# Kernel optimization log

Hardware: AMD Instinct MI355X
Metric: run time of the kernel (lower is better)

Reference implementation:

```python
import jax, jax.numpy as jnp
import numpy as np

NHEAD = 16
HEAD_DIM = 64
EMBED_DIM = NHEAD * HEAD_DIM  # 1024
U, R, L, M = 2048, 256, 1024, 512


def setup_inputs() -> dict:
    key = jax.random.key(0)
    ks = jax.random.split(key, 11)
    D = EMBED_DIM
    inp = {
        "utterance": jax.random.normal(ks[0], (U, 1, D), jnp.float32),
        "right_context": jax.random.normal(ks[1], (R, 1, D), jnp.float32),
        "memory": jax.random.normal(ks[2], (M, 1, D), jnp.float32),
        "left_context_key": jax.random.normal(ks[3], (L, 1, D), jnp.float32),
        "left_context_val": jax.random.normal(ks[4], (L, 1, D), jnp.float32),
        "Wq": jax.random.normal(ks[5], (D, D), jnp.float32) * 0.02,
        "bq": jax.random.normal(ks[6], (D,), jnp.float32) * 0.02,
        "Wkv": jax.random.normal(ks[7], (2 * D, D), jnp.float32) * 0.02,
        "bkv": jax.random.normal(ks[8], (2 * D,), jnp.float32) * 0.02,
        "Wo": jax.random.normal(ks[9], (D, D), jnp.float32) * 0.02,
        "bo": jax.random.normal(ks[10], (D,), jnp.float32) * 0.02,
    }
    return inp


def reference(utterance, right_context, memory, left_context_key, left_context_val,
              Wq, bq, Wkv, bkv, Wo, bo):
    D = EMBED_DIM
    scaling = HEAD_DIM ** (-0.5)

    # query = Linear([right_context; utterance])  -> (Q, 1, D), Q = R + U
    q_in = jnp.concatenate([right_context, utterance], axis=0)
    query = q_in @ Wq.T + bq

    # key/value = Linear([memory; right_context; utterance]) split in two
    kv_in = jnp.concatenate([memory, right_context, utterance], axis=0)
    kv = kv_in @ Wkv.T + bkv  # (M+R+U, 1, 2D)
    k_new, v_new = kv[..., :D], kv[..., D:]

    # insert cached left-context key/value after [memory; right_context]
    key = jnp.concatenate([k_new[: M + R], left_context_key, k_new[M + R:]], axis=0)
    value = jnp.concatenate([v_new[: M + R], left_context_val, v_new[M + R:]], axis=0)

    Q = U + R
    KV = M + R + L + U
    # (T, 1, D) -> (nhead, T, head_dim)
    q = query.reshape(Q, NHEAD, HEAD_DIM).transpose(1, 0, 2)
    k = key.reshape(KV, NHEAD, HEAD_DIM).transpose(1, 0, 2)
    v = value.reshape(KV, NHEAD, HEAD_DIM).transpose(1, 0, 2)

    weights = jnp.einsum("hqd,hkd->hqk", q * scaling, k)  # (nhead, Q, KV)
    probs = jax.nn.softmax(weights, axis=-1)
    attn = jnp.einsum("hqk,hkd->hqd", probs, v)  # (nhead, Q, head_dim)

    attn = attn.transpose(1, 0, 2).reshape(Q, D)[:, None, :]  # (Q, 1, D)
    out = attn @ Wo.T + bo
    return out, key, value
```

## Files before the change

kernel.cpp:

```cpp
#include <hip/hip_runtime.h>
#include <hip/hip_bf16.h>

#define EMBED   1024
#define NHEADS  16
#define HDIM    64
#define U_LEN   2048
#define R_LEN   256
#define L_LEN   1024
#define M_LEN   512
#define Q_LEN   (U_LEN + R_LEN)
#define KV_LEN  (M_LEN + R_LEN + L_LEN + U_LEN)
#define X_ROWS  (M_LEN + R_LEN + U_LEN)
#define NPART   6
#define KV_PART (KV_LEN / NPART)

typedef __attribute__((ext_vector_type(8))) short short8;
typedef __attribute__((ext_vector_type(4))) float f32x4;
typedef __attribute__((ext_vector_type(16))) float f32x16;

#define QSCALE 0.180336880f

__device__ __forceinline__ void gl2lds16(const __hip_bfloat16* g, __hip_bfloat16* l) {
  __builtin_amdgcn_global_load_lds(
      (const __attribute__((address_space(1))) unsigned int*)g,
      (__attribute__((address_space(3))) unsigned int*)l, 16, 0, 0);
}

__device__ __forceinline__ unsigned pack_bf16(float a, float b) {
  unsigned ua = __builtin_bit_cast(unsigned, a) + 0x8000u;
  unsigned ub = __builtin_bit_cast(unsigned, b) + 0x8000u;
  return (ua >> 16) | (ub & 0xFFFF0000u);
}

__global__ __launch_bounds__(256) void prep_kernel(
    const float* __restrict__ mem, const float* __restrict__ rc,
    const float* __restrict__ utt, const float* __restrict__ lk,
    const float* __restrict__ lv, const float* __restrict__ Wq,
    const float* __restrict__ Wkv, const float* __restrict__ Wo,
    __hip_bfloat16* __restrict__ X, __hip_bfloat16* __restrict__ WB,
    __hip_bfloat16* __restrict__ WoB,
    float* __restrict__ key_out, float* __restrict__ val_out,
    __hip_bfloat16* __restrict__ k_bf, __hip_bfloat16* __restrict__ v_bf) {
  int b = blockIdx.x, tid = threadIdx.x;
  if (b < 2816) {
    int row = b, col = tid * 4;
    const float* src;
    if (row < M_LEN)              src = mem + row * EMBED;
    else if (row < M_LEN + R_LEN) src = rc + (row - M_LEN) * EMBED;
    else                          src = utt + (row - M_LEN - R_LEN) * EMBED;
    float4 v = *reinterpret_cast<const float4*>(src + col);
    __hip_bfloat16* d = X + (size_t)row * EMBED + col;
    d[0] = __float2bfloat16(v.x); d[1] = __float2bfloat16(v.y);
    d[2] = __float2bfloat16(v.z); d[3] = __float2bfloat16(v.w);
  } else if (b < 6912) {
    const float* src; __hip_bfloat16* dst;
    int blk;
    if (b < 3840)      { src = Wq;  dst = WB;                blk = b - 2816; }
    else if (b < 5888) { src = Wkv; dst = WB + 1024 * 1024;  blk = b - 3840; }
    else               { src = Wo;  dst = WoB;               blk = b - 5888; }
    int idx = blk * 1024 + tid * 4;
    float4 v = *reinterpret_cast<const float4*>(src + idx);
    dst[idx + 0] = __float2bfloat16(v.x);
    dst[idx + 1] = __float2bfloat16(v.y);
    dst[idx + 2] = __float2bfloat16(v.z);
    dst[idx + 3] = __float2bfloat16(v.w);
  } else {
    int row = b - 6912, c0 = tid * 4;
    int orow = 768 + row;
    float4 kv4 = *reinterpret_cast<const float4*>(lk + row * EMBED + c0);
    float4 vv4 = *reinterpret_cast<const float4*>(lv + row * EMBED + c0);
    *reinterpret_cast<float4*>(key_out + (size_t)orow * EMBED + c0) = kv4;
    *reinterpret_cast<float4*>(val_out + (size_t)orow * EMBED + c0) = vv4;
    __hip_bfloat16* kd = k_bf + (size_t)orow * EMBED + c0;
    __hip_bfloat16* vd = v_bf + (size_t)orow * EMBED + c0;
    kd[0] = __float2bfloat16(kv4.x); kd[1] = __float2bfloat16(kv4.y);
    kd[2] = __float2bfloat16(kv4.z); kd[3] = __float2bfloat16(kv4.w);
    vd[0] = __float2bfloat16(vv4.x); vd[1] = __float2bfloat16(vv4.y);
    vd[2] = __float2bfloat16(vv4.z); vd[3] = __float2bfloat16(vv4.w);
  }
}

__global__ __launch_bounds__(256) void transpose_kernel(
    const unsigned short* __restrict__ v_bf, unsigned short* __restrict__ vT) {
  __shared__ unsigned short T[64][72];
  int kt = blockIdx.x * 64, d0 = blockIdx.y * 64;
  int t = threadIdx.x;
  int r = t >> 3, c = (t & 7) * 8;
#pragma unroll
  for (int half = 0; half < 2; half++) {
    int kv = r + half * 32;
    short8 v = *reinterpret_cast<const short8*>(v_bf + (size_t)(kt + kv) * EMBED + d0 + c);
#pragma unroll
    for (int j = 0; j < 8; j++) T[c + j][kv] = (unsigned short)v[j];
  }
  __syncthreads();
#pragma unroll
  for (int half = 0; half < 2; half++) {
    int d = r + half * 32;
    *reinterpret_cast<short8*>(vT + (size_t)(d0 + d) * KV_LEN + kt + c) =
        *reinterpret_cast<const short8*>(&T[d][c]);
  }
}

__global__ __launch_bounds__(256) void gemm_qkv(
    const __hip_bfloat16* __restrict__ A, const __hip_bfloat16* __restrict__ B,
    const float* __restrict__ bq, const float* __restrict__ bkv,
    float* __restrict__ key_out, float* __restrict__ val_out,
    __hip_bfloat16* __restrict__ q_bf, __hip_bfloat16* __restrict__ k_bf,
    __hip_bfloat16* __restrict__ v_bf) {
  __shared__ __align__(16) __hip_bfloat16 As[128 * 32];
  __shared__ __align__(16) __hip_bfloat16 Bs[128 * 32];
  const int K = EMBED;
  int tid = threadIdx.x;
  int wave = tid >> 6, lane = tid & 63, quad = lane >> 4, l16 = lane & 15;
  int wm = wave >> 1, wn = wave & 1;
  int mbase = blockIdx.y * 128, nbase = blockIdx.x * 128;

  if (nbase < 1024 && mbase + 128 <= 512) return;

  const __hip_bfloat16* a0 = A + (size_t)(mbase + (tid >> 2)) * K + (tid & 3) * 8;
  const __hip_bfloat16* a1 = a0 + (size_t)64 * K;
  const __hip_bfloat16* b0 = B + (size_t)(nbase + (tid >> 2)) * K + (tid & 3) * 8;
  const __hip_bfloat16* b1 = b0 + (size_t)64 * K;
  __hip_bfloat16* lA0 = As + tid * 8;
  __hip_bfloat16* lA1 = As + (tid + 256) * 8;
  __hip_bfloat16* lB0 = Bs + tid * 8;
  __hip_bfloat16* lB1 = Bs + (tid + 256) * 8;

  f32x4 acc[4][4] = {};
  for (int kt = 0; kt < K; kt += 32) {
    gl2lds16(a0 + kt, lA0);
    gl2lds16(a1 + kt, lA1);
    gl2lds16(b0 + kt, lB0);
    gl2lds16(b1 + kt, lB1);
    __syncthreads();
    short8 af[4], bfr[4];
#pragma unroll
    for (int i = 0; i < 4; i++)
      af[i] = *reinterpret_cast<const short8*>(As + (wm * 64 + i * 16 + l16) * 32 + quad * 8);
#pragma unroll
    for (int j = 0; j < 4; j++)
      bfr[j] = *reinterpret_cast<const short8*>(Bs + (wn * 64 + j * 16 + l16) * 32 + quad * 8);
#pragma unroll
    for (int i = 0; i < 4; i++)
#pragma unroll
      for (int j = 0; j < 4; j++)
        acc[i][j] = __builtin_amdgcn_mfma_f32_16x16x32_bf16(af[i], bfr[j], acc[i][j], 0, 0, 0);
    __syncthreads();
  }

#pragma unroll
  for (int i = 0; i < 4; i++) {
    int rb = mbase + wm * 64 + i * 16 + quad * 4;
#pragma unroll
    for (int j = 0; j < 4; j++) {
      int cg = nbase + wn * 64 + j * 16 + l16;
      float bv = (cg < 1024) ? bq[cg] : bkv[cg - 1024];
#pragma unroll
      for (int reg = 0; reg < 4; reg++) {
        int rg = rb + reg;
        float val = acc[i][j][reg] + bv;
        if (cg < 1024) {
          if (rg >= 512)
            q_bf[(size_t)(rg - 512) * 1024 + cg] = __float2bfloat16(val * QSCALE);
        } else {
          int orow = (rg < 768) ? rg : rg + 1024;
          if (cg < 2048) {
            int cc = cg - 1024;
            key_out[(size_t)orow * 1024 + cc] = val;
            k_bf[(size_t)orow * 1024 + cc] = __float2bfloat16(val);
          } else {
            int cc = cg - 2048;
            val_out[(size_t)orow * 1024 + cc] = val;
            v_bf[(size_t)orow * 1024 + cc] = __float2bfloat16(val);
          }
        }
      }
    }
  }
}

__global__ __launch_bounds__(256) void gemm_out(
    const __hip_bfloat16* __restrict__ A, const __hip_bfloat16* __restrict__ B,
    const float* __restrict__ bias, float* __restrict__ outf) {
  __shared__ __align__(16) __hip_bfloat16 As[64 * 32];
  __shared__ __align__(16) __hip_bfloat16 Bs[128 * 32];
  const int K = EMBED, N = EMBED;
  int tid = threadIdx.x;
  int wave = tid >> 6, lane = tid & 63, quad = lane >> 4, l16 = lane & 15;
  int wm = wave >> 1, wn = wave & 1;
  int mbase = blockIdx.y * 64, nbase = blockIdx.x * 128;

  const __hip_bfloat16* a0 = A + (size_t)(mbase + (tid >> 2)) * K + (tid & 3) * 8;
  const __hip_bfloat16* b0 = B + (size_t)(nbase + (tid >> 2)) * K + (tid & 3) * 8;
  const __hip_bfloat16* b1 = b0 + (size_t)64 * K;
  __hip_bfloat16* lA0 = As + tid * 8;
  __hip_bfloat16* lB0 = Bs + tid * 8;
  __hip_bfloat16* lB1 = Bs + (tid + 256) * 8;

  f32x4 acc[2][4] = {};
  for (int kt = 0; kt < K; kt += 32) {
    gl2lds16(a0 + kt, lA0);
    gl2lds16(b0 + kt, lB0);
    gl2lds16(b1 + kt, lB1);
    __syncthreads();
    short8 af[2], bfr[4];
#pragma unroll
    for (int i = 0; i < 2; i++)
      af[i] = *reinterpret_cast<const short8*>(As + (wm * 32 + i * 16 + l16) * 32 + quad * 8);
#pragma unroll
    for (int j = 0; j < 4; j++)
      bfr[j] = *reinterpret_cast<const short8*>(Bs + (wn * 64 + j * 16 + l16) * 32 + quad * 8);
#pragma unroll
    for (int i = 0; i < 2; i++)
#pragma unroll
      for (int j = 0; j < 4; j++)
        acc[i][j] = __builtin_amdgcn_mfma_f32_16x16x32_bf16(af[i], bfr[j], acc[i][j], 0, 0, 0);
    __syncthreads();
  }

#pragma unroll
  for (int i = 0; i < 2; i++) {
    int rb = mbase + wm * 32 + i * 16 + quad * 4;
#pragma unroll
    for (int j = 0; j < 4; j++) {
      int cg = nbase + wn * 64 + j * 16 + l16;
      float bv = bias[cg];
#pragma unroll
      for (int reg = 0; reg < 4; reg++)
        outf[(size_t)(rb + reg) * N + cg] = acc[i][j][reg] + bv;
    }
  }
}

__global__ __launch_bounds__(256, 4) void attn_kernel(
    const __hip_bfloat16* __restrict__ q_bf, const __hip_bfloat16* __restrict__ k_bf,
    const __hip_bfloat16* __restrict__ vT,
    __hip_bfloat16* __restrict__ o_part, float* __restrict__ lsum) {
  __shared__ __align__(16) __hip_bfloat16 Ks[64][72];
  __shared__ __align__(16) __hip_bfloat16 VTs[64][72];
  int tid = threadIdx.x;
  int w = tid >> 6, lane = tid & 63, l31 = lane & 31, h2 = lane >> 5;
  int h = blockIdx.y, part = blockIdx.z;
  int qbase = blockIdx.x * 128;
  int qg = qbase + w * 32 + l31;

  short8 Qf[4];
#pragma unroll
  for (int ks = 0; ks < 4; ks++)
    Qf[ks] = *reinterpret_cast<const short8*>(
        q_bf + (size_t)qg * EMBED + h * HDIM + ks * 16 + h2 * 8);

  f32x16 ot[2] = {};
  float l_run = 0.f;

  int sr = tid >> 3, sc = (tid & 7) * 8;
  const int kv0 = part * KV_PART;

  for (int kt = kv0; kt < kv0 + KV_PART; kt += 64) {
#pragma unroll
    for (int half = 0; half < 2; half++) {
      int r = sr + half * 32;
      *reinterpret_cast<short8*>(&Ks[r][sc]) =
          *reinterpret_cast<const short8*>(k_bf + (size_t)(kt + r) * EMBED + h * HDIM + sc);
      *reinterpret_cast<short8*>(&VTs[r][sc]) =
          *reinterpret_cast<const short8*>(vT + (size_t)(h * HDIM + r) * KV_LEN + kt + sc);
    }
    __syncthreads();

#pragma unroll
    for (int kvs = 0; kvs < 2; kvs++) {
      f32x16 s = {};
#pragma unroll
      for (int ks = 0; ks < 4; ks++) {
        short8 ak = *reinterpret_cast<const short8*>(&Ks[kvs * 32 + l31][ks * 16 + h2 * 8]);
        s = __builtin_amdgcn_mfma_f32_32x32x16_bf16(ak, Qf[ks], s, 0, 0, 0);
      }
      unsigned u[4][2];
#pragma unroll
      for (int g = 0; g < 4; g++) {
        float p0 = exp2f(s[4 * g + 0]), p1 = exp2f(s[4 * g + 1]);
        float p2 = exp2f(s[4 * g + 2]), p3 = exp2f(s[4 * g + 3]);
        l_run += (p0 + p1) + (p2 + p3);
        u[g][0] = pack_bf16(p0, p1);
        u[g][1] = pack_bf16(p2, p3);
      }
#pragma unroll
      for (int half = 0; half < 2; half++) {
        int c = kvs * 2 + half;
        int gA = 2 * half, gB = 2 * half + 1;
        unsigned s0 = h2 ? u[gA][0] : u[gB][0];
        unsigned s1 = h2 ? u[gA][1] : u[gB][1];
        unsigned r0 = __shfl_xor(s0, 32, 64);
        unsigned r1 = __shfl_xor(s1, 32, 64);
        uint4 fr;
        fr.x = h2 ? r0 : u[gA][0];
        fr.y = h2 ? r1 : u[gA][1];
        fr.z = h2 ? u[gB][0] : r0;
        fr.w = h2 ? u[gB][1] : r1;
        short8 pf = __builtin_bit_cast(short8, fr);
#pragma unroll
        for (int ds = 0; ds < 2; ds++) {
          short8 av = *reinterpret_cast<const short8*>(&VTs[ds * 32 + l31][c * 16 + h2 * 8]);
          ot[ds] = __builtin_amdgcn_mfma_f32_32x32x16_bf16(av, pf, ot[ds], 0, 0, 0);
        }
      }
    }
    __syncthreads();
  }

  l_run += __shfl_xor(l_run, 32, 64);
  float inv = 1.0f / l_run;

  size_t orow = (size_t)part * Q_LEN + qg;
#pragma unroll
  for (int ds = 0; ds < 2; ds++)
#pragma unroll
    for (int g = 0; g < 4; g++) {
      uint2 pk;
      pk.x = pack_bf16(ot[ds][4 * g + 0] * inv, ot[ds][4 * g + 1] * inv);
      pk.y = pack_bf16(ot[ds][4 * g + 2] * inv, ot[ds][4 * g + 3] * inv);
      *reinterpret_cast<uint2*>(
          o_part + orow * 1024 + h * HDIM + ds * 32 + g * 8 + h2 * 4) = pk;
    }
  if (lane < 32)
    lsum[orow * NHEADS + h] = l_run;
}

__global__ __launch_bounds__(256) void merge_kernel(
    const __hip_bfloat16* __restrict__ o_part, const float* __restrict__ lsum,
    __hip_bfloat16* __restrict__ attn_bf) {
  int q = blockIdx.x;
  int c = threadIdx.x * 4;
  int h = c >> 6;
  float wt[NPART], L = 0.f;
#pragma unroll
  for (int p = 0; p < NPART; p++) {
    wt[p] = lsum[((size_t)p * Q_LEN + q) * NHEADS + h];
    L += wt[p];
  }
  float invL = 1.0f / L;
  float acc[4] = {0.f, 0.f, 0.f, 0.f};
#pragma unroll
  for (int p = 0; p < NPART; p++) {
    __hip_bfloat16 v[4];
    *reinterpret_cast<uint2*>(v) =
        *reinterpret_cast<const uint2*>(o_part + ((size_t)p * Q_LEN + q) * 1024 + c);
#pragma unroll
    for (int j = 0; j < 4; j++) acc[j] += wt[p] * __bfloat162float(v[j]);
  }
  uint2 pk;
  pk.x = pack_bf16(acc[0] * invL, acc[1] * invL);
  pk.y = pack_bf16(acc[2] * invL, acc[3] * invL);
  *reinterpret_cast<uint2*>(attn_bf + (size_t)q * 1024 + c) = pk;
}


extern "C" void kernel_launch(void* const* d_in, const int* in_sizes, int n_in,
                              void* d_out, int out_size, void* d_ws, size_t ws_size,
                              hipStream_t stream) {
  const float* utt = (const float*)d_in[0];
  const float* rc  = (const float*)d_in[1];
  const float* mem = (const float*)d_in[2];
  const float* lk  = (const float*)d_in[3];
  const float* lv  = (const float*)d_in[4];
  const float* Wq  = (const float*)d_in[5];
  const float* bq  = (const float*)d_in[6];
  const float* Wkv = (const float*)d_in[7];
  const float* bkv = (const float*)d_in[8];
  const float* Wo  = (const float*)d_in[9];
  const float* bo  = (const float*)d_in[10];

  float* out_f   = (float*)d_out;
  float* key_out = out_f + Q_LEN * EMBED;
  float* val_out = key_out + KV_LEN * EMBED;

  char* ws = (char*)d_ws;
  size_t off = 0;
  __hip_bfloat16* X_bf   = (__hip_bfloat16*)(ws + off); off += (size_t)X_ROWS * EMBED * 2;
  __hip_bfloat16* WB_bf  = (__hip_bfloat16*)(ws + off); off += (size_t)3 * EMBED * EMBED * 2;
  __hip_bfloat16* Wo_bf  = (__hip_bfloat16*)(ws + off); off += (size_t)EMBED * EMBED * 2;
  __hip_bfloat16* q_bf   = (__hip_bfloat16*)(ws + off); off += (size_t)Q_LEN * EMBED * 2;
  __hip_bfloat16* k_bf   = (__hip_bfloat16*)(ws + off); off += (size_t)KV_LEN * EMBED * 2;
  __hip_bfloat16* vT_bf  = (__hip_bfloat16*)(ws + off); off += (size_t)EMBED * KV_LEN * 2;
  __hip_bfloat16* o_part = (__hip_bfloat16*)(ws + off); off += (size_t)NPART * Q_LEN * EMBED * 2;
  __hip_bfloat16* attn_bf = X_bf;
  float* lsum = (float*)WB_bf;
  __hip_bfloat16* v_bf = o_part;
  (void)off; (void)ws_size; (void)in_sizes; (void)n_in; (void)out_size;

  prep_kernel<<<7936, 256, 0, stream>>>(mem, rc, utt, lk, lv, Wq, Wkv, Wo,
                                        X_bf, WB_bf, Wo_bf,
                                        key_out, val_out, k_bf, v_bf);
  gemm_qkv<<<dim3(3 * EMBED / 128, X_ROWS / 128), 256, 0, stream>>>(
      X_bf, WB_bf, bq, bkv, key_out, val_out, q_bf, k_bf, v_bf);
  transpose_kernel<<<dim3(KV_LEN / 64, EMBED / 64), 256, 0, stream>>>(
      (const unsigned short*)v_bf, (unsigned short*)vT_bf);
  attn_kernel<<<dim3(Q_LEN / 128, NHEADS, NPART), 256, 0, stream>>>(
      q_bf, k_bf, vT_bf, o_part, lsum);
  merge_kernel<<<Q_LEN, 256, 0, stream>>>(o_part, lsum, attn_bf);
  gemm_out<<<dim3(EMBED / 128, Q_LEN / 64), 256, 0, stream>>>(
      attn_bf, Wo_bf, bo, out_f);
}
```

Before: 243.0 us.

## Retile GEMMs with BK=64 XOR-swizzled LDS and split-K output projection

```diff
diff --git a/kernel.cpp b/kernel.cpp
--- a/kernel.cpp
+++ b/kernel.cpp
@@ -108,44 +108,48 @@
     float* __restrict__ key_out, float* __restrict__ val_out,
     __hip_bfloat16* __restrict__ q_bf, __hip_bfloat16* __restrict__ k_bf,
     __hip_bfloat16* __restrict__ v_bf) {
-  __shared__ __align__(16) __hip_bfloat16 As[128 * 32];
-  __shared__ __align__(16) __hip_bfloat16 Bs[128 * 32];
+  __shared__ __align__(16) __hip_bfloat16 As[128 * 64];
+  __shared__ __align__(16) __hip_bfloat16 Bs[64 * 64];
   const int K = EMBED;
   int tid = threadIdx.x;
   int wave = tid >> 6, lane = tid & 63, quad = lane >> 4, l16 = lane & 15;
   int wm = wave >> 1, wn = wave & 1;
-  int mbase = blockIdx.y * 128, nbase = blockIdx.x * 128;
+  int mbase = blockIdx.y * 128, nbase = blockIdx.x * 64;
 
   if (nbase < 1024 && mbase + 128 <= 512) return;
 
-  const __hip_bfloat16* a0 = A + (size_t)(mbase + (tid >> 2)) * K + (tid & 3) * 8;
-  const __hip_bfloat16* a1 = a0 + (size_t)64 * K;
-  const __hip_bfloat16* b0 = B + (size_t)(nbase + (tid >> 2)) * K + (tid & 3) * 8;
-  const __hip_bfloat16* b1 = b0 + (size_t)64 * K;
-  __hip_bfloat16* lA0 = As + tid * 8;
-  __hip_bfloat16* lA1 = As + (tid + 256) * 8;
-  __hip_bfloat16* lB0 = Bs + tid * 8;
-  __hip_bfloat16* lB1 = Bs + (tid + 256) * 8;
-
-  f32x4 acc[4][4] = {};
-  for (int kt = 0; kt < K; kt += 32) {
-    gl2lds16(a0 + kt, lA0);
-    gl2lds16(a1 + kt, lA1);
-    gl2lds16(b0 + kt, lB0);
-    gl2lds16(b1 + kt, lB1);
-    __syncthreads();
-    short8 af[4], bfr[4];
-#pragma unroll
-    for (int i = 0; i < 4; i++)
-      af[i] = *reinterpret_cast<const short8*>(As + (wm * 64 + i * 16 + l16) * 32 + quad * 8);
-#pragma unroll
-    for (int j = 0; j < 4; j++)
-      bfr[j] = *reinterpret_cast<const short8*>(Bs + (wn * 64 + j * 16 + l16) * 32 + quad * 8);
-#pragma unroll
-    for (int i = 0; i < 4; i++)
-#pragma unroll
-      for (int j = 0; j < 4; j++)
-        acc[i][j] = __builtin_amdgcn_mfma_f32_16x16x32_bf16(af[i], bfr[j], acc[i][j], 0, 0, 0);
+  int srow = tid >> 3;
+  int scol = ((tid & 7) ^ (srow & 7)) * 8;
+  const __hip_bfloat16* aG = A + (size_t)(mbase + srow) * K + scol;
+  const __hip_bfloat16* bG = B + (size_t)(nbase + srow) * K + scol;
+  int swz = l16 & 7;
+
+  f32x4 acc[4][2] = {};
+  for (int kt = 0; kt < K; kt += 64) {
+    gl2lds16(aG + kt, As + tid * 8);
+    gl2lds16(aG + (size_t)32 * K + kt, As + (tid + 256) * 8);
+    gl2lds16(aG + (size_t)64 * K + kt, As + (tid + 512) * 8);
+    gl2lds16(aG + (size_t)96 * K + kt, As + (tid + 768) * 8);
+    gl2lds16(bG + kt, Bs + tid * 8);
+    gl2lds16(bG + (size_t)32 * K + kt, Bs + (tid + 256) * 8);
+    __syncthreads();
+#pragma unroll
+    for (int ks = 0; ks < 2; ks++) {
+      short8 af[4], bfr[2];
+#pragma unroll
+      for (int i = 0; i < 4; i++)
+        af[i] = *reinterpret_cast<const short8*>(
+            As + (wm * 64 + i * 16 + l16) * 64 + ((ks * 4 + quad) ^ swz) * 8);
+#pragma unroll
+      for (int j = 0; j < 2; j++)
+        bfr[j] = *reinterpret_cast<const short8*>(
+            Bs + (wn * 32 + j * 16 + l16) * 64 + ((ks * 4 + quad) ^ swz) * 8);
+#pragma unroll
+      for (int i = 0; i < 4; i++)
+#pragma unroll
+        for (int j = 0; j < 2; j++)
+          acc[i][j] = __builtin_amdgcn_mfma_f32_16x16x32_bf16(af[i], bfr[j], acc[i][j], 0, 0, 0);
+    }
     __syncthreads();
   }
 
@@ -153,8 +157,8 @@
   for (int i = 0; i < 4; i++) {
     int rb = mbase + wm * 64 + i * 16 + quad * 4;
 #pragma unroll
-    for (int j = 0; j < 4; j++) {
-      int cg = nbase + wn * 64 + j * 16 + l16;
+    for (int j = 0; j < 2; j++) {
+      int cg = nbase + wn * 32 + j * 16 + l16;
       float bv = (cg < 1024) ? bq[cg] : bkv[cg - 1024];
 #pragma unroll
       for (int reg = 0; reg < 4; reg++) {
@@ -182,40 +186,47 @@
 
 __global__ __launch_bounds__(256) void gemm_out(
     const __hip_bfloat16* __restrict__ A, const __hip_bfloat16* __restrict__ B,
-    const float* __restrict__ bias, float* __restrict__ outf) {
-  __shared__ __align__(16) __hip_bfloat16 As[64 * 32];
-  __shared__ __align__(16) __hip_bfloat16 Bs[128 * 32];
+    float* __restrict__ partial) {
+  __shared__ __align__(16) __hip_bfloat16 As[64 * 64];
+  __shared__ __align__(16) __hip_bfloat16 Bs[64 * 64];
   const int K = EMBED, N = EMBED;
   int tid = threadIdx.x;
   int wave = tid >> 6, lane = tid & 63, quad = lane >> 4, l16 = lane & 15;
   int wm = wave >> 1, wn = wave & 1;
-  int mbase = blockIdx.y * 64, nbase = blockIdx.x * 128;
-
-  const __hip_bfloat16* a0 = A + (size_t)(mbase + (tid >> 2)) * K + (tid & 3) * 8;
-  const __hip_bfloat16* b0 = B + (size_t)(nbase + (tid >> 2)) * K + (tid & 3) * 8;
-  const __hip_bfloat16* b1 = b0 + (size_t)64 * K;
-  __hip_bfloat16* lA0 = As + tid * 8;
-  __hip_bfloat16* lB0 = Bs + tid * 8;
-  __hip_bfloat16* lB1 = Bs + (tid + 256) * 8;
-
-  f32x4 acc[2][4] = {};
-  for (int kt = 0; kt < K; kt += 32) {
-    gl2lds16(a0 + kt, lA0);
-    gl2lds16(b0 + kt, lB0);
-    gl2lds16(b1 + kt, lB1);
-    __syncthreads();
-    short8 af[2], bfr[4];
-#pragma unroll
-    for (int i = 0; i < 2; i++)
-      af[i] = *reinterpret_cast<const short8*>(As + (wm * 32 + i * 16 + l16) * 32 + quad * 8);
-#pragma unroll
-    for (int j = 0; j < 4; j++)
-      bfr[j] = *reinterpret_cast<const short8*>(Bs + (wn * 64 + j * 16 + l16) * 32 + quad * 8);
-#pragma unroll
-    for (int i = 0; i < 2; i++)
-#pragma unroll
-      for (int j = 0; j < 4; j++)
-        acc[i][j] = __builtin_amdgcn_mfma_f32_16x16x32_bf16(af[i], bfr[j], acc[i][j], 0, 0, 0);
+  int mbase = blockIdx.y * 64, nbase = blockIdx.x * 64;
+  int kbase = blockIdx.z * 512;
+  float* outp = partial + (size_t)blockIdx.z * Q_LEN * EMBED;
+
+  int srow = tid >> 3;
+  int scol = ((tid & 7) ^ (srow & 7)) * 8;
+  const __hip_bfloat16* aG = A + (size_t)(mbase + srow) * K + kbase + scol;
+  const __hip_bfloat16* bG = B + (size_t)(nbase + srow) * K + kbase + scol;
+  int swz = l16 & 7;
+
+  f32x4 acc[2][2] = {};
+  for (int kt = 0; kt < 512; kt += 64) {
+    gl2lds16(aG + kt, As + tid * 8);
+    gl2lds16(aG + (size_t)32 * K + kt, As + (tid + 256) * 8);
+    gl2lds16(bG + kt, Bs + tid * 8);
+    gl2lds16(bG + (size_t)32 * K + kt, Bs + (tid + 256) * 8);
+    __syncthreads();
+#pragma unroll
+    for (int ks = 0; ks < 2; ks++) {
+      short8 af[2], bfr[2];
+#pragma unroll
+      for (int i = 0; i < 2; i++)
+        af[i] = *reinterpret_cast<const short8*>(
+            As + (wm * 32 + i * 16 + l16) * 64 + ((ks * 4 + quad) ^ swz) * 8);
+#pragma unroll
+      for (int j = 0; j < 2; j++)
+        bfr[j] = *reinterpret_cast<const short8*>(
+            Bs + (wn * 32 + j * 16 + l16) * 64 + ((ks * 4 + quad) ^ swz) * 8);
+#pragma unroll
+      for (int i = 0; i < 2; i++)
+#pragma unroll
+        for (int j = 0; j < 2; j++)
+          acc[i][j] = __builtin_amdgcn_mfma_f32_16x16x32_bf16(af[i], bfr[j], acc[i][j], 0, 0, 0);
+    }
     __syncthreads();
   }
 
@@ -223,14 +234,26 @@
   for (int i = 0; i < 2; i++) {
     int rb = mbase + wm * 32 + i * 16 + quad * 4;
 #pragma unroll
-    for (int j = 0; j < 4; j++) {
-      int cg = nbase + wn * 64 + j * 16 + l16;
-      float bv = bias[cg];
+    for (int j = 0; j < 2; j++) {
+      int cg = nbase + wn * 32 + j * 16 + l16;
 #pragma unroll
       for (int reg = 0; reg < 4; reg++)
-        outf[(size_t)(rb + reg) * N + cg] = acc[i][j][reg] + bv;
-    }
-  }
+        outp[(size_t)(rb + reg) * N + cg] = acc[i][j][reg];
+    }
+  }
+}
+
+__global__ __launch_bounds__(256) void reduce_out_kernel(
+    const float* __restrict__ partial, const float* __restrict__ bias,
+    float* __restrict__ outf) {
+  int row = blockIdx.x, c = threadIdx.x * 4;
+  float4 p0 = *reinterpret_cast<const float4*>(partial + (size_t)row * EMBED + c);
+  float4 p1 = *reinterpret_cast<const float4*>(partial + (size_t)(Q_LEN + row) * EMBED + c);
+  float4 bv = *reinterpret_cast<const float4*>(bias + c);
+  float4 o;
+  o.x = p0.x + p1.x + bv.x; o.y = p0.y + p1.y + bv.y;
+  o.z = p0.z + p1.z + bv.z; o.w = p0.w + p1.w + bv.w;
+  *reinterpret_cast<float4*>(outf + (size_t)row * EMBED + c) = o;
 }
 
 __global__ __launch_bounds__(256, 4) void attn_kernel(
@@ -387,18 +410,20 @@
   __hip_bfloat16* attn_bf = X_bf;
   float* lsum = (float*)WB_bf;
   __hip_bfloat16* v_bf = o_part;
+  float* out_partial = (float*)q_bf;
   (void)off; (void)ws_size; (void)in_sizes; (void)n_in; (void)out_size;
 
   prep_kernel<<<7936, 256, 0, stream>>>(mem, rc, utt, lk, lv, Wq, Wkv, Wo,
                                         X_bf, WB_bf, Wo_bf,
                                         key_out, val_out, k_bf, v_bf);
-  gemm_qkv<<<dim3(3 * EMBED / 128, X_ROWS / 128), 256, 0, stream>>>(
+  gemm_qkv<<<dim3(3 * EMBED / 64, X_ROWS / 128), 256, 0, stream>>>(
       X_bf, WB_bf, bq, bkv, key_out, val_out, q_bf, k_bf, v_bf);
   transpose_kernel<<<dim3(KV_LEN / 64, EMBED / 64), 256, 0, stream>>>(
       (const unsigned short*)v_bf, (unsigned short*)vT_bf);
   attn_kernel<<<dim3(Q_LEN / 128, NHEADS, NPART), 256, 0, stream>>>(
       q_bf, k_bf, vT_bf, o_part, lsum);
   merge_kernel<<<Q_LEN, 256, 0, stream>>>(o_part, lsum, attn_bf);
-  gemm_out<<<dim3(EMBED / 128, Q_LEN / 64), 256, 0, stream>>>(
-      attn_bf, Wo_bf, bo, out_f);
-}
+  gemm_out<<<dim3(EMBED / 64, Q_LEN / 64, 2), 256, 0, stream>>>(
+      attn_bf, Wo_bf, out_partial);
+  reduce_out_kernel<<<Q_LEN, 256, 0, stream>>>(out_partial, bo, out_f);
+}
```

Result: faster. 237.7 us (-2.2%).
